# Performance work log

Hardware: AMD Instinct MI355X
Metric: run time of the kernel (lower is better)

The kernel has to match this reference:

```python
import jax, jax.numpy as jnp
import numpy as np

D_MODEL = 1024
N_HEADS = 8
HEAD_DIM = D_MODEL // N_HEADS
B, T = 4, 2048


def setup_inputs() -> dict:
    key = jax.random.key(0)
    ks = jax.random.split(key, 10)
    x = jax.random.normal(ks[0], (B, T, D_MODEL), dtype=jnp.float32)
    # causal mask: True entries are masked (matches torch masked_fill semantics)
    mask = jnp.triu(jnp.ones((T, T), dtype=bool), k=1)

    def xavier(k, shape):
        fan_in, fan_out = shape[1], shape[0]
        lim = float(np.sqrt(6.0 / (fan_in + fan_out)))
        return jax.random.uniform(k, shape, jnp.float32, -lim, lim)

    Wq = xavier(ks[1], (D_MODEL, D_MODEL)); bq = jnp.zeros((D_MODEL,), jnp.float32)
    Wk = xavier(ks[2], (D_MODEL, D_MODEL)); bk = jnp.zeros((D_MODEL,), jnp.float32)
    Wv = xavier(ks[3], (D_MODEL, D_MODEL)); bv = jnp.zeros((D_MODEL,), jnp.float32)
    Wo = xavier(ks[4], (D_MODEL, D_MODEL)); bo = jnp.zeros((D_MODEL,), jnp.float32)
    return {"x": x, "mask": mask, "Wq": Wq, "bq": bq, "Wk": Wk, "bk": bk,
            "Wv": Wv, "bv": bv, "Wo": Wo, "bo": bo}


def reference(x, mask, Wq, bq, Wk, bk, Wv, bv, Wo, bo):
    Bsz, Tlen, _ = x.shape
    # torch Linear: y = x @ W.T + b
    Q = (x @ Wq.T + bq).reshape(Bsz, Tlen, N_HEADS, HEAD_DIM).transpose(0, 2, 1, 3)  # [B,H,T,Dh]
    K = (x @ Wk.T + bk).reshape(Bsz, Tlen, N_HEADS, HEAD_DIM).transpose(0, 2, 1, 3)  # [B,H,T,Dh]
    V_shared = x @ Wv.T + bv  # [B,T,D] shared across heads
    scale = 1.0 / jnp.sqrt(jnp.float32(HEAD_DIM))
    scores = jnp.einsum('bhqd,bhkd->bhqk', Q, K) * scale  # [B,H,T,T]
    scores = jnp.where(mask[None, None, :, :], jnp.float32(-1e9), scores)
    attn_per_head = jax.nn.softmax(scores, axis=-1)
    alpha_agg = attn_per_head.mean(axis=1)  # [B,T,T] head-averaged attention
    out = jnp.einsum('bqk,bkd->bqd', alpha_agg, V_shared) @ Wo.T + bo
    return out, alpha_agg
```

## Files before the change

kernel.cpp:

```cpp
#include <hip/hip_runtime.h>
#include <hip/hip_bf16.h>

#define D_MODEL 1024
#define NH 8
#define HD 128
#define BATCH 4
#define TSEQ 2048
#define MROWS (BATCH * TSEQ)
#define QKV_LD 3072
#define SBAND 131072

typedef __attribute__((ext_vector_type(8))) __bf16 bf16x8;
typedef __attribute__((ext_vector_type(4))) __bf16 bf16x4;
typedef __attribute__((ext_vector_type(4))) float f32x4;
typedef __attribute__((ext_vector_type(8))) unsigned short u16x8;

#define SC2 0.1275174441680632f

__device__ __forceinline__ void gload16(const void* g, void* lds) {
  __builtin_amdgcn_global_load_lds(
      (const __attribute__((address_space(1))) unsigned int*)g,
      (__attribute__((address_space(3))) unsigned int*)lds, 16, 0, 0);
}

__global__ __launch_bounds__(256) void cvt_f32_to_bf16(const float* __restrict__ in,
                                                       __bf16* __restrict__ out, int n4) {
  int i = blockIdx.x * 256 + threadIdx.x;
  if (i < n4) {
    float4 v = reinterpret_cast<const float4*>(in)[i];
    bf16x4 o;
    o[0] = (__bf16)v.x; o[1] = (__bf16)v.y; o[2] = (__bf16)v.z; o[3] = (__bf16)v.w;
    reinterpret_cast<bf16x4*>(out)[i] = o;
  }
}

__global__ __launch_bounds__(256) void cvt4_weights(const float* __restrict__ w0,
                                                    const float* __restrict__ w1,
                                                    const float* __restrict__ w2,
                                                    const float* __restrict__ w3,
                                                    __bf16* __restrict__ out) {
  const int per = D_MODEL * D_MODEL / 4;
  int i = blockIdx.x * 256 + threadIdx.x;
  int m = i / per, j = i - m * per;
  const float* src = (m == 0) ? w0 : (m == 1) ? w1 : (m == 2) ? w2 : w3;
  float4 v = reinterpret_cast<const float4*>(src)[j];
  bf16x4 o;
  o[0] = (__bf16)v.x; o[1] = (__bf16)v.y; o[2] = (__bf16)v.z; o[3] = (__bf16)v.w;
  reinterpret_cast<bf16x4*>(out)[i] = o;
}

__global__ __launch_bounds__(256) void concat_bias(const float* __restrict__ a,
                                                   const float* __restrict__ b,
                                                   const float* __restrict__ c,
                                                   float* __restrict__ o) {
  int i = blockIdx.x * 256 + threadIdx.x;
  if (i < 3072) o[i] = (i < 1024) ? a[i] : (i < 2048) ? b[i - 1024] : c[i - 2048];
}

__global__ __launch_bounds__(256) void invert_lsum(float* __restrict__ L, int n) {
  int i = blockIdx.x * 256 + threadIdx.x;
  if (i < n) L[i] = 1.0f / (8.0f * L[i]);
}

template <bool BF16OUT, bool CAUSAL, bool AFP32>
__global__ __launch_bounds__(256) void gemm128(const void* __restrict__ Aip,
                                               const __bf16* __restrict__ Bp,
                                               const float* __restrict__ bias,
                                               void* __restrict__ Yp, int K, int ldy,
                                               size_t sA, size_t sB, size_t sY) {
  __shared__ __bf16 As[2][128 * 32];
  __shared__ __bf16 Bs[2][128 * 32];
  const int tid = threadIdx.x;
  const int w = tid >> 6, l = tid & 63;
  const int lr = l & 15, lg = l >> 4;
  const int m0 = blockIdx.y * 128, n0 = blockIdx.x * 128;
  const int z = blockIdx.z;
  const __bf16* Ab = AFP32 ? nullptr : (const __bf16*)Aip + z * sA;
  const float* Af = AFP32 ? (const float*)Aip + z * sA : nullptr;
  const __bf16* Bb = Bp + z * sB;
  const int wm = w >> 1, wn = w & 1;
  f32x4 acc[4][4] = {};
  const int Klim = CAUSAL ? (m0 + 128 < K ? m0 + 128 : K) : K;
  const int nt = Klim >> 5;

  auto stage = [&](int t, int buf) {
    const int k0 = t << 5;
    if constexpr (!AFP32) {
#pragma unroll
      for (int i = 0; i < 2; ++i) {
        int s = w * 128 + i * 64 + l;
        int row = s >> 2, scp = s & 3;
        int sc = scp ^ ((row >> 1) & 3);
        gload16(Ab + (size_t)(m0 + row) * K + k0 + sc * 8, (char*)As[buf] + s * 16);
      }
    } else {
#pragma unroll
      for (int i = 0; i < 2; ++i) {
        int s = w * 128 + i * 64 + l;
        int row = s >> 2, sc = s & 3;
        const float* src = Af + (size_t)(m0 + row) * K + k0 + sc * 8;
        float4 lo = *reinterpret_cast<const float4*>(src);
        float4 hi = *reinterpret_cast<const float4*>(src + 4);
        bf16x8 v;
        v[0] = (__bf16)lo.x; v[1] = (__bf16)lo.y; v[2] = (__bf16)lo.z; v[3] = (__bf16)lo.w;
        v[4] = (__bf16)hi.x; v[5] = (__bf16)hi.y; v[6] = (__bf16)hi.z; v[7] = (__bf16)hi.w;
        int p = row * 4 + (sc ^ ((row >> 1) & 3));
        *reinterpret_cast<bf16x8*>((char*)As[buf] + p * 16) = v;
      }
    }
#pragma unroll
    for (int i = 0; i < 2; ++i) {
      int s = w * 128 + i * 64 + l;
      int row = s >> 2, scp = s & 3;
      int sc = scp ^ ((row >> 1) & 3);
      gload16(Bb + (size_t)(n0 + row) * K + k0 + sc * 8, (char*)Bs[buf] + s * 16);
    }
  };

  stage(0, 0);
  __syncthreads();
  int cur = 0;
  for (int t = 0; t < nt; ++t) {
    if (t + 1 < nt) stage(t + 1, cur ^ 1);
    bf16x8 af[4], bf[4];
#pragma unroll
    for (int f = 0; f < 4; ++f) {
      int ar = wm * 64 + f * 16 + lr;
      af[f] = *reinterpret_cast<const bf16x8*>((const char*)As[cur] + ar * 64 +
                                               ((lg ^ ((ar >> 1) & 3)) * 16));
      int br = wn * 64 + f * 16 + lr;
      bf[f] = *reinterpret_cast<const bf16x8*>((const char*)Bs[cur] + br * 64 +
                                               ((lg ^ ((br >> 1) & 3)) * 16));
    }
#pragma unroll
    for (int mf = 0; mf < 4; ++mf)
#pragma unroll
      for (int nf = 0; nf < 4; ++nf)
        acc[mf][nf] = __builtin_amdgcn_mfma_f32_16x16x32_bf16(af[mf], bf[nf], acc[mf][nf], 0, 0, 0);
    __syncthreads();
    cur ^= 1;
  }

#pragma unroll
  for (int mf = 0; mf < 4; ++mf) {
#pragma unroll
    for (int nf = 0; nf < 4; ++nf) {
#pragma unroll
      for (int r = 0; r < 4; ++r) {
        int grow = m0 + wm * 64 + mf * 16 + lg * 4 + r;
        int gcol = n0 + wn * 64 + nf * 16 + lr;
        float v = acc[mf][nf][r];
        if (bias) v += bias[gcol];
        if constexpr (BF16OUT)
          ((__bf16*)Yp + z * sY)[(size_t)grow * ldy + gcol] = (__bf16)v;
        else
          ((float*)Yp + z * sY)[(size_t)grow * ldy + gcol] = v;
      }
    }
  }
}

__global__ __launch_bounds__(256) void transpose_v(const __bf16* __restrict__ V,
                                                   __bf16* __restrict__ Vt) {
  __shared__ unsigned short tile[64 * 72];
  const int b = blockIdx.z;
  const int t0 = blockIdx.x * 64, d0 = blockIdx.y * 64;
  const int tid = threadIdx.x;
#pragma unroll
  for (int i = 0; i < 2; ++i) {
    int s = i * 256 + tid;
    int r = s >> 3, c8 = s & 7;
    u16x8 v = *reinterpret_cast<const u16x8*>(V + ((size_t)b * TSEQ + t0 + r) * QKV_LD + d0 + c8 * 8);
    *reinterpret_cast<u16x8*>(&tile[r * 72 + c8 * 8]) = v;
  }
  __syncthreads();
#pragma unroll
  for (int i = 0; i < 2; ++i) {
    int s = i * 256 + tid;
    int dr = s >> 3, t8 = s & 7;
    u16x8 o;
#pragma unroll
    for (int j = 0; j < 8; ++j) o[j] = tile[(t8 * 8 + j) * 72 + dr];
    *reinterpret_cast<u16x8*>(Vt + ((size_t)b * D_MODEL + d0 + dr) * TSEQ + t0 + t8 * 8) = o;
  }
}

__global__ __launch_bounds__(256) void score_gemm(const __bf16* __restrict__ QKV,
                                                  __bf16* __restrict__ S,
                                                  float* __restrict__ lsum, int b) {
  __shared__ __bf16 As[2][128 * 32];
  __shared__ __bf16 Bs[2][128 * 32];
  const int tid = threadIdx.x;
  const int w = tid >> 6, l = tid & 63;
  const int lr = l & 15, lg = l >> 4;
  const int wm = w >> 1, wn = w & 1;
  const int idx = blockIdx.x;
  const int h = blockIdx.y;
  int qt = (int)((sqrtf(8.f * (float)idx + 1.f) - 1.f) * 0.5f);
  while ((qt + 1) * (qt + 2) / 2 <= idx) ++qt;
  while (qt * (qt + 1) / 2 > idx) --qt;
  const int kt = idx - qt * (qt + 1) / 2;
  const int q0 = qt * 128, k0 = kt * 128;
  const int kext = (qt + 1) * 128;
  const bool diag = (kt == qt);

  const __bf16* Ab = QKV + (size_t)(b * TSEQ + q0) * QKV_LD + h * HD;
  const __bf16* Bb = QKV + (size_t)(b * TSEQ + k0) * QKV_LD + 1024 + h * HD;

  auto stage = [&](int t, int buf) {
#pragma unroll
    for (int i = 0; i < 2; ++i) {
      int s = w * 128 + i * 64 + l;
      int row = s >> 2, scp = s & 3;
      int sc = scp ^ ((row >> 1) & 3);
      gload16(Ab + (size_t)row * QKV_LD + t * 32 + sc * 8, (char*)As[buf] + s * 16);
    }
#pragma unroll
    for (int i = 0; i < 2; ++i) {
      int s = w * 128 + i * 64 + l;
      int row = s >> 2, scp = s & 3;
      int sc = scp ^ ((row >> 1) & 3);
      gload16(Bb + (size_t)row * QKV_LD + t * 32 + sc * 8, (char*)Bs[buf] + s * 16);
    }
  };

  f32x4 acc[4][4] = {};
  stage(0, 0);
  __syncthreads();
  int cur = 0;
#pragma unroll
  for (int t = 0; t < 4; ++t) {
    if (t < 3) stage(t + 1, cur ^ 1);
    bf16x8 af[4], bf[4];
#pragma unroll
    for (int f = 0; f < 4; ++f) {
      int ar = wm * 64 + f * 16 + lr;
      af[f] = *reinterpret_cast<const bf16x8*>((const char*)As[cur] + ar * 64 +
                                               ((lg ^ ((ar >> 1) & 3)) * 16));
      int br = wn * 64 + f * 16 + lr;
      bf[f] = *reinterpret_cast<const bf16x8*>((const char*)Bs[cur] + br * 64 +
                                               ((lg ^ ((br >> 1) & 3)) * 16));
    }
#pragma unroll
    for (int mf = 0; mf < 4; ++mf)
#pragma unroll
      for (int nf = 0; nf < 4; ++nf)
        acc[mf][nf] = __builtin_amdgcn_mfma_f32_16x16x32_bf16(af[mf], bf[nf], acc[mf][nf], 0, 0, 0);
    __syncthreads();
    cur ^= 1;
  }

  __bf16* Sb = S + (size_t)SBAND * ((qt * (qt + 1)) >> 1) + (size_t)h * 128 * kext + k0;
  float ls[4][4] = {};
#pragma unroll
  for (int mf = 0; mf < 4; ++mf) {
#pragma unroll
    for (int r = 0; r < 4; ++r) {
      int row = wm * 64 + mf * 16 + lg * 4 + r;
      __bf16* srow = Sb + (size_t)row * kext;
#pragma unroll
      for (int nf = 0; nf < 4; ++nf) {
        int col = wn * 64 + nf * 16 + lr;
        float v = acc[mf][nf][r];
        srow[col] = (__bf16)v;
        if (!diag || col <= row) ls[mf][r] += exp2f(v * SC2);
      }
    }
  }
#pragma unroll
  for (int m = 1; m < 16; m <<= 1)
#pragma unroll
    for (int mf = 0; mf < 4; ++mf)
#pragma unroll
      for (int r = 0; r < 4; ++r) ls[mf][r] += __shfl_xor(ls[mf][r], m, 64);
  if (lr == 0) {
#pragma unroll
    for (int mf = 0; mf < 4; ++mf)
#pragma unroll
      for (int r = 0; r < 4; ++r)
        atomicAdd(&lsum[((size_t)(b * NH + h)) * TSEQ + q0 + wm * 64 + mf * 16 + lg * 4 + r],
                  ls[mf][r]);
  }
}

__global__ __launch_bounds__(256) void alpha_stream(const __bf16* __restrict__ S,
                                                    const float* __restrict__ Linv,
                                                    float* __restrict__ alpha, int b) {
  const int q = blockIdx.x;
  const int qt = q >> 7;
  const int kext = (qt + 1) * 128;
  const int k0 = threadIdx.x * 8;
  float* arow = alpha + ((size_t)(b * TSEQ + q)) * TSEQ + k0;
  if (k0 >= kext) {
    float4 zz = {0.f, 0.f, 0.f, 0.f};
    *reinterpret_cast<float4*>(arow) = zz;
    *reinterpret_cast<float4*>(arow + 4) = zz;
    return;
  }
  const __bf16* Sb = S + (size_t)SBAND * ((qt * (qt + 1)) >> 1) + (size_t)(q & 127) * kext + k0;
  const size_t hstride = (size_t)128 * kext;
  float o[8] = {};
#pragma unroll
  for (int h = 0; h < NH; ++h) {
    float li = Linv[((size_t)(b * NH + h)) * TSEQ + q];
    bf16x8 s8 = *reinterpret_cast<const bf16x8*>(Sb + h * hstride);
#pragma unroll
    for (int j = 0; j < 8; ++j) o[j] += exp2f((float)s8[j] * SC2) * li;
  }
#pragma unroll
  for (int j = 0; j < 8; ++j)
    if (k0 + j > q) o[j] = 0.f;
  float4 lo = {o[0], o[1], o[2], o[3]};
  float4 hi = {o[4], o[5], o[6], o[7]};
  *reinterpret_cast<float4*>(arow) = lo;
  *reinterpret_cast<float4*>(arow + 4) = hi;
}

extern "C" void kernel_launch(void* const* d_in, const int* in_sizes, int n_in,
                              void* d_out, int out_size, void* d_ws, size_t ws_size,
                              hipStream_t stream) {
  const float* x  = (const float*)d_in[0];
  const float* Wq = (const float*)d_in[2];
  const float* bq = (const float*)d_in[3];
  const float* Wk = (const float*)d_in[4];
  const float* bk = (const float*)d_in[5];
  const float* Wv = (const float*)d_in[6];
  const float* bv = (const float*)d_in[7];
  const float* Wo = (const float*)d_in[8];
  const float* bo = (const float*)d_in[9];

  float* out_f = (float*)d_out;
  float* alpha = out_f + (size_t)MROWS * D_MODEL;

  char* p = (char*)d_ws;
  __bf16* xb   = (__bf16*)p; p += (size_t)MROWS * D_MODEL * 2;
  __bf16* wqb  = (__bf16*)p; p += (size_t)D_MODEL * D_MODEL * 2;
  __bf16* wkb  = (__bf16*)p; p += (size_t)D_MODEL * D_MODEL * 2;
  __bf16* wvb  = (__bf16*)p; p += (size_t)D_MODEL * D_MODEL * 2;
  __bf16* wob  = (__bf16*)p; p += (size_t)D_MODEL * D_MODEL * 2;
  __bf16* qkv  = (__bf16*)p; p += (size_t)MROWS * QKV_LD * 2;
  __bf16* vtb  = (__bf16*)p; p += (size_t)BATCH * D_MODEL * TSEQ * 2;
  float* lsum  = (float*)p;  p += (size_t)BATCH * NH * TSEQ * 4;
  __bf16* sbuf = (__bf16*)p; p += (size_t)SBAND * 136 * 2;
  float* bcat  = (float*)p;  p += 3072 * 4;
  __bf16* midb = xb;

  hipMemsetAsync(lsum, 0, (size_t)BATCH * NH * TSEQ * 4, stream);

  {
    int n4 = MROWS * D_MODEL / 4;
    cvt_f32_to_bf16<<<n4 / 256, 256, 0, stream>>>(x, xb, n4);
    int w4 = 4 * D_MODEL * D_MODEL / 4;
    cvt4_weights<<<w4 / 256, 256, 0, stream>>>(Wq, Wk, Wv, Wo, wqb);
    concat_bias<<<12, 256, 0, stream>>>(bq, bk, bv, bcat);
  }

  gemm128<true, false, false><<<dim3(QKV_LD / 128, MROWS / 128), 256, 0, stream>>>(
      xb, wqb, bcat, qkv, D_MODEL, QKV_LD, 0, 0, 0);

  transpose_v<<<dim3(TSEQ / 64, D_MODEL / 64, BATCH), 256, 0, stream>>>(qkv + 2048, vtb);

  for (int b = 0; b < BATCH; ++b) {
    score_gemm<<<dim3(136, NH), 256, 0, stream>>>(qkv, sbuf, lsum, b);
    invert_lsum<<<(NH * TSEQ) / 256, 256, 0, stream>>>(lsum + (size_t)b * NH * TSEQ, NH * TSEQ);
    alpha_stream<<<TSEQ, 256, 0, stream>>>(sbuf, lsum, alpha, b);
  }

  gemm128<true, true, true><<<dim3(D_MODEL / 128, TSEQ / 128, BATCH), 256, 0, stream>>>(
      alpha, vtb, nullptr, midb, TSEQ, D_MODEL,
      (size_t)TSEQ * TSEQ, (size_t)D_MODEL * TSEQ, (size_t)TSEQ * D_MODEL);

  gemm128<false, false, false><<<dim3(D_MODEL / 128, MROWS / 128), 256, 0, stream>>>(
      midb, wob, bo, out_f, D_MODEL, D_MODEL, 0, 0, 0);
}
```

Baseline: 368.8 us.

## Batch score/alpha launches across batches, fold lsum inversion, add XCD-aware grid swizzle

```diff
diff --git a/kernel.cpp b/kernel.cpp
--- a/kernel.cpp
+++ b/kernel.cpp
@@ -9,6 +9,7 @@
 #define MROWS (BATCH * TSEQ)
 #define QKV_LD 3072
 #define SBAND 131072
+#define SBATCH ((size_t)SBAND * 136)
 
 typedef __attribute__((ext_vector_type(8))) __bf16 bf16x8;
 typedef __attribute__((ext_vector_type(4))) __bf16 bf16x4;
@@ -21,6 +22,20 @@
   __builtin_amdgcn_global_load_lds(
       (const __attribute__((address_space(1))) unsigned int*)g,
       (__attribute__((address_space(3))) unsigned int*)lds, 16, 0, 0);
+}
+
+__device__ __forceinline__ dim3 swz_grid() {
+  const int nx = gridDim.x, ny = gridDim.y;
+  const int nwg = nx * ny * gridDim.z;
+  int L = blockIdx.x + nx * (blockIdx.y + ny * blockIdx.z);
+  const int q = nwg >> 3, r = nwg & 7;
+  const int xcd = L & 7, idx = L >> 3;
+  int t = (xcd < r ? xcd * (q + 1) : r * (q + 1) + (xcd - r) * q) + idx;
+  dim3 o;
+  o.x = t % nx; t /= nx;
+  o.y = t % ny;
+  o.z = t / ny;
+  return o;
 }
 
 __global__ __launch_bounds__(256) void cvt_f32_to_bf16(const float* __restrict__ in,
@@ -57,11 +72,6 @@
   if (i < 3072) o[i] = (i < 1024) ? a[i] : (i < 2048) ? b[i - 1024] : c[i - 2048];
 }
 
-__global__ __launch_bounds__(256) void invert_lsum(float* __restrict__ L, int n) {
-  int i = blockIdx.x * 256 + threadIdx.x;
-  if (i < n) L[i] = 1.0f / (8.0f * L[i]);
-}
-
 template <bool BF16OUT, bool CAUSAL, bool AFP32>
 __global__ __launch_bounds__(256) void gemm128(const void* __restrict__ Aip,
                                                const __bf16* __restrict__ Bp,
@@ -70,11 +80,12 @@
                                                size_t sA, size_t sB, size_t sY) {
   __shared__ __bf16 As[2][128 * 32];
   __shared__ __bf16 Bs[2][128 * 32];
+  const dim3 bi = swz_grid();
   const int tid = threadIdx.x;
   const int w = tid >> 6, l = tid & 63;
   const int lr = l & 15, lg = l >> 4;
-  const int m0 = blockIdx.y * 128, n0 = blockIdx.x * 128;
-  const int z = blockIdx.z;
+  const int m0 = bi.y * 128, n0 = bi.x * 128;
+  const int z = bi.z;
   const __bf16* Ab = AFP32 ? nullptr : (const __bf16*)Aip + z * sA;
   const float* Af = AFP32 ? (const float*)Aip + z * sA : nullptr;
   const __bf16* Bb = Bp + z * sB;
@@ -187,15 +198,19 @@
 
 __global__ __launch_bounds__(256) void score_gemm(const __bf16* __restrict__ QKV,
                                                   __bf16* __restrict__ S,
-                                                  float* __restrict__ lsum, int b) {
+                                                  float* __restrict__ lsum,
+                                                  int b0, size_t sstride) {
   __shared__ __bf16 As[2][128 * 32];
   __shared__ __bf16 Bs[2][128 * 32];
+  const dim3 bi = swz_grid();
   const int tid = threadIdx.x;
   const int w = tid >> 6, l = tid & 63;
   const int lr = l & 15, lg = l >> 4;
   const int wm = w >> 1, wn = w & 1;
-  const int idx = blockIdx.x;
-  const int h = blockIdx.y;
+  const int idx = bi.x;
+  const int h = bi.y;
+  const int zz = bi.z;
+  const int b = b0 + zz;
   int qt = (int)((sqrtf(8.f * (float)idx + 1.f) - 1.f) * 0.5f);
   while ((qt + 1) * (qt + 2) / 2 <= idx) ++qt;
   while (qt * (qt + 1) / 2 > idx) --qt;
@@ -250,7 +265,8 @@
     cur ^= 1;
   }
 
-  __bf16* Sb = S + (size_t)SBAND * ((qt * (qt + 1)) >> 1) + (size_t)h * 128 * kext + k0;
+  __bf16* Sb = S + zz * sstride + (size_t)SBAND * ((qt * (qt + 1)) >> 1) +
+               (size_t)h * 128 * kext + k0;
   float ls[4][4] = {};
 #pragma unroll
   for (int mf = 0; mf < 4; ++mf) {
@@ -284,25 +300,29 @@
 }
 
 __global__ __launch_bounds__(256) void alpha_stream(const __bf16* __restrict__ S,
-                                                    const float* __restrict__ Linv,
-                                                    float* __restrict__ alpha, int b) {
+                                                    const float* __restrict__ lsum,
+                                                    float* __restrict__ alpha,
+                                                    int b0, size_t sstride) {
   const int q = blockIdx.x;
+  const int zz = blockIdx.y;
+  const int b = b0 + zz;
   const int qt = q >> 7;
   const int kext = (qt + 1) * 128;
   const int k0 = threadIdx.x * 8;
   float* arow = alpha + ((size_t)(b * TSEQ + q)) * TSEQ + k0;
   if (k0 >= kext) {
-    float4 zz = {0.f, 0.f, 0.f, 0.f};
-    *reinterpret_cast<float4*>(arow) = zz;
-    *reinterpret_cast<float4*>(arow + 4) = zz;
+    float4 zzf = {0.f, 0.f, 0.f, 0.f};
+    *reinterpret_cast<float4*>(arow) = zzf;
+    *reinterpret_cast<float4*>(arow + 4) = zzf;
     return;
   }
-  const __bf16* Sb = S + (size_t)SBAND * ((qt * (qt + 1)) >> 1) + (size_t)(q & 127) * kext + k0;
+  const __bf16* Sb = S + zz * sstride + (size_t)SBAND * ((qt * (qt + 1)) >> 1) +
+                     (size_t)(q & 127) * kext + k0;
   const size_t hstride = (size_t)128 * kext;
   float o[8] = {};
 #pragma unroll
   for (int h = 0; h < NH; ++h) {
-    float li = Linv[((size_t)(b * NH + h)) * TSEQ + q];
+    float li = 1.0f / (8.0f * lsum[((size_t)(b * NH + h)) * TSEQ + q]);
     bf16x8 s8 = *reinterpret_cast<const bf16x8*>(Sb + h * hstride);
 #pragma unroll
     for (int j = 0; j < 8; ++j) o[j] += exp2f((float)s8[j] * SC2) * li;
@@ -341,9 +361,16 @@
   __bf16* qkv  = (__bf16*)p; p += (size_t)MROWS * QKV_LD * 2;
   __bf16* vtb  = (__bf16*)p; p += (size_t)BATCH * D_MODEL * TSEQ * 2;
   float* lsum  = (float*)p;  p += (size_t)BATCH * NH * TSEQ * 4;
-  __bf16* sbuf = (__bf16*)p; p += (size_t)SBAND * 136 * 2;
   float* bcat  = (float*)p;  p += 3072 * 4;
+  __bf16* sbuf = (__bf16*)p;
   __bf16* midb = xb;
+
+  size_t used = (size_t)((char*)sbuf - (char*)d_ws);
+  size_t sb1 = SBATCH * 2;
+  int NB = 1;
+  if (ws_size >= used + 4 * sb1) NB = 4;
+  else if (ws_size >= used + 2 * sb1) NB = 2;
+  size_t sstride = (NB > 1) ? SBATCH : 0;
 
   hipMemsetAsync(lsum, 0, (size_t)BATCH * NH * TSEQ * 4, stream);
 
@@ -360,10 +387,9 @@
 
   transpose_v<<<dim3(TSEQ / 64, D_MODEL / 64, BATCH), 256, 0, stream>>>(qkv + 2048, vtb);
 
-  for (int b = 0; b < BATCH; ++b) {
-    score_gemm<<<dim3(136, NH), 256, 0, stream>>>(qkv, sbuf, lsum, b);
-    invert_lsum<<<(NH * TSEQ) / 256, 256, 0, stream>>>(lsum + (size_t)b * NH * TSEQ, NH * TSEQ);
-    alpha_stream<<<TSEQ, 256, 0, stream>>>(sbuf, lsum, alpha, b);
+  for (int b0 = 0; b0 < BATCH; b0 += NB) {
+    score_gemm<<<dim3(136, NH, NB), 256, 0, stream>>>(qkv, sbuf, lsum, b0, sstride);
+    alpha_stream<<<dim3(TSEQ, NB), 256, 0, stream>>>(sbuf, lsum, alpha, b0, sstride);
   }
 
   gemm128<true, true, true><<<dim3(D_MODEL / 128, TSEQ / 128, BATCH), 256, 0, stream>>>(
```

Result: no change. 363.3 us (-1.5%).
